# Kernel tuning notes

Hardware: AMD Instinct MI355X
Metric: run time of the kernel (lower is better)

Reference implementation:

```python
import jax, jax.numpy as jnp
import numpy as np
from jax.scipy.linalg import solve_triangular

EPS = 2e-05  # module eps (only used on Cholesky failure in torch; cov is PD here since M >> N)


def setup_inputs() -> dict:
    key = jax.random.key(0)
    k1, k2, k3 = jax.random.split(key, 3)
    B, N, H, W = 8, 512, 64, 64
    return {
        "cont_feat": jax.random.normal(k1, (B, N, H, W), dtype=jnp.float32),
        "styl_feat": jax.random.normal(k2, (B, N, H, W), dtype=jnp.float32),
        "x_real": jax.random.normal(k3, (B, N, H, W), dtype=jnp.float32),
    }


def reference(cont_feat, styl_feat, x_real):
    B, N, cH, cW = cont_feat.shape
    xc = cont_feat.reshape(B, N, -1)   # [B, N, Mc]
    xs = styl_feat.reshape(B, N, -1)   # [B, N, Ms]
    # x_real is reshaped in the original but never used by whitening()

    # whitening: center, covariance, Cholesky, inv(L) @ x (as triangular solve)
    xc_c = xc - jnp.mean(xc, axis=-1, keepdims=True)
    cov_c = jnp.einsum('bnm,bkm->bnk', xc_c, xc_c) / (xc_c.shape[-1] - 1)  # [B,N,N]
    Lc = jnp.linalg.cholesky(cov_c)
    whiten = solve_triangular(Lc, xc_c, lower=True)  # == inv(Lc) @ xc_c

    # coloring: style covariance Cholesky, Ls @ whiten + style mean
    xs_mean = jnp.mean(xs, axis=-1, keepdims=True)
    xs_c = xs - xs_mean
    cov_s = jnp.einsum('bnm,bkm->bnk', xs_c, xs_c) / (xs_c.shape[-1] - 1)
    Ls = jnp.linalg.cholesky(cov_s)
    out = jnp.einsum('bnk,bkm->bnm', Ls, whiten) + xs_mean
    return out.reshape(B, N, cH, cW)
```

## Files before the change

### kernel.cpp

```cpp
#include <hip/hip_runtime.h>
#include <stdint.h>


using short8   = __attribute__((ext_vector_type(8))) short;
using short4_t = __attribute__((ext_vector_type(4))) short;
using f32x4    = __attribute__((ext_vector_type(4))) float;

#define DEVI static __device__ __forceinline__

DEVI uint16_t f32_to_bf16(float f) {
  union { float f; uint32_t u; } v{f};
  uint32_t u = v.u;
  return (uint16_t)((u + 0x7fffu + ((u >> 16) & 1u)) >> 16);
}

DEVI f32x4 mfma16(short8 a, short8 b, f32x4 c) {
  return __builtin_amdgcn_mfma_f32_16x16x32_bf16(a, b, c, 0, 0, 0);
}

typedef __attribute__((address_space(3))) uint32_t lds_u32;
typedef __attribute__((address_space(1))) const uint32_t gmem_u32;

DEVI void async_cp16(const uint16_t* g, uint16_t* l) {
  __builtin_amdgcn_global_load_lds((gmem_u32*)g, (lds_u32*)l, 16, 0, 0);
}

DEVI void stage_tile(const uint16_t* __restrict__ src, int stride,
                     uint16_t* lds, int tid) {
  int w64 = (tid >> 6) << 6;
  #pragma unroll
  for (int i = 0; i < 4; ++i) {
    int f = i * 256 + tid;
    int r = f >> 3, s = f & 7;
    int c = s ^ (r & 7);
    async_cp16(src + r * stride + c * 8, lds + (i * 256 + w64) * 8);
  }
}

DEVI short8 frag_ld(const uint16_t* lds, int r, int ch) {
  return *(const short8*)(lds + r * 64 + ((ch ^ (r & 7)) * 8));
}

__global__ __launch_bounds__(256) void k_meanconv(
    const float* __restrict__ cont, const float* __restrict__ styl,
    uint16_t* __restrict__ Yc, uint16_t* __restrict__ Ys, float* __restrict__ mus) {
  int rid = blockIdx.x;
  int row = rid & 4095;
  bool is_s = rid >= 4096;
  const float* src = (is_s ? styl : cont) + (size_t)row * 4096;
  uint16_t* dst = (is_s ? Ys : Yc) + (size_t)row * 4096;
  int tid = threadIdx.x, lane = tid & 63, w = tid >> 6;

  float4 v[4];
  #pragma unroll
  for (int i = 0; i < 4; ++i) v[i] = ((const float4*)src)[i * 256 + tid];
  float s = 0.f;
  #pragma unroll
  for (int i = 0; i < 4; ++i) s += v[i].x + v[i].y + v[i].z + v[i].w;
  #pragma unroll
  for (int off = 32; off > 0; off >>= 1) s += __shfl_down(s, off);
  __shared__ float red[4];
  if (lane == 0) red[w] = s;
  __syncthreads();
  float mean = (red[0] + red[1] + red[2] + red[3]) * (1.0f / 4096.0f);
  if (is_s && tid == 0) mus[row] = mean;

  #pragma unroll
  for (int i = 0; i < 4; ++i) {
    short4_t o;
    o[0] = (short)f32_to_bf16(v[i].x - mean);
    o[1] = (short)f32_to_bf16(v[i].y - mean);
    o[2] = (short)f32_to_bf16(v[i].z - mean);
    o[3] = (short)f32_to_bf16(v[i].w - mean);
    ((short4_t*)dst)[i * 256 + tid] = o;
  }
}

__global__ __launch_bounds__(256) void k_cov(const uint16_t* __restrict__ Y,
                                             float* __restrict__ covA) {
  int bx = blockIdx.x;
  int mat = bx / 10, q = bx % 10;
  int it = (q >= 6) ? 3 : (q >= 3) ? 2 : (q >= 1) ? 1 : 0;
  int jt = q - it * (it + 1) / 2;
  const uint16_t* A = Y + (size_t)mat * 2097152;
  float* C = covA + (size_t)mat * 262144;
  __shared__ uint16_t Al[128 * 64], Bl[128 * 64];
  int tid = threadIdx.x, lane = tid & 63, w = tid >> 6;
  int wr = w >> 1, wc = w & 1, m16 = lane & 15, q4 = lane >> 4;

  f32x4 acc[4][4] = {};
  for (int kb = 0; kb < 64; ++kb) {
    __syncthreads();
    stage_tile(A + it * 128 * 4096 + kb * 64, 4096, Al, tid);
    stage_tile(A + jt * 128 * 4096 + kb * 64, 4096, Bl, tid);
    __syncthreads();
    #pragma unroll
    for (int ks = 0; ks < 2; ++ks) {
      short8 af[4], bg[4];
      #pragma unroll
      for (int t = 0; t < 4; ++t) af[t] = frag_ld(Al, wr * 64 + t * 16 + m16, ks * 4 + q4);
      #pragma unroll
      for (int t = 0; t < 4; ++t) bg[t] = frag_ld(Bl, wc * 64 + t * 16 + m16, ks * 4 + q4);
      #pragma unroll
      for (int i2 = 0; i2 < 4; ++i2)
        #pragma unroll
        for (int j2 = 0; j2 < 4; ++j2)
          acc[i2][j2] = mfma16(af[i2], bg[j2], acc[i2][j2]);
    }
  }
  const float sc = 1.0f / 4095.0f;
  #pragma unroll
  for (int t = 0; t < 4; ++t)
    #pragma unroll
    for (int u = 0; u < 4; ++u)
      #pragma unroll
      for (int g = 0; g < 4; ++g) {
        int row = it * 128 + wr * 64 + t * 16 + q4 * 4 + g;
        int col = jt * 128 + wc * 64 + u * 16 + m16;
        C[row * 512 + col] = acc[t][u][g] * sc;
      }
}

__global__ __launch_bounds__(512) void k_chol(float* __restrict__ covA,
                                              uint16_t* __restrict__ L16) {
  int mat = blockIdx.x;
  float* C = covA + (size_t)mat * 262144;
  uint16_t* L = L16 + (size_t)mat * 262144;
  __shared__ float P[512 * 33];
  __shared__ float invD[32];
  int tid = threadIdx.x, lane = tid & 63, w = tid >> 6;
  int m16 = lane & 15, q4 = lane >> 4;

  for (int j = 0; j < 16; ++j) {
    int c0 = j * 32, n = 512 - c0;
    for (int e = tid; e < n * 32; e += 512) {
      int r = e >> 5, c = e & 31;
      P[r * 33 + c] = C[(c0 + r) * 512 + c0 + c];
    }
    __syncthreads();
    if (j > 0) {
      int ntiles = n >> 4;
      for (int t = w; t < ntiles; t += 8) {
        f32x4 acc0 = {}, acc1 = {};
        for (int kk = 0; kk < c0; kk += 32) {
          short8 a  = *(const short8*)(L + (size_t)(c0 + t * 16 + m16) * 512 + kk + q4 * 8);
          short8 b0 = *(const short8*)(L + (size_t)(c0 + m16) * 512 + kk + q4 * 8);
          short8 b1 = *(const short8*)(L + (size_t)(c0 + 16 + m16) * 512 + kk + q4 * 8);
          acc0 = mfma16(a, b0, acc0);
          acc1 = mfma16(a, b1, acc1);
        }
        #pragma unroll
        for (int g = 0; g < 4; ++g) {
          int r = t * 16 + q4 * 4 + g;
          P[r * 33 + m16]      -= acc0[g];
          P[r * 33 + 16 + m16] -= acc1[g];
        }
      }
    }
    __syncthreads();
    if (w == 0 && lane < 32) {
      int r = lane;
      float a[32];
      #pragma unroll
      for (int c = 0; c < 32; ++c) a[c] = P[r * 33 + c];
      #pragma unroll
      for (int t = 0; t < 32; ++t) {
        float pv  = __shfl(a[t], t);
        float inv = __builtin_amdgcn_rsqf(pv);
        a[t] *= inv;
        if (r == 0) invD[t] = inv;
        float scv = a[t];
        #pragma unroll
        for (int c = t + 1; c < 32; ++c)
          a[c] -= scv * __shfl(scv, c);
      }
      #pragma unroll
      for (int c = 0; c < 32; ++c) P[r * 33 + c] = a[c];
    }
    __syncthreads();
    if (n > 32) {
      int r = 32 + tid;
      if (r < n) {
        float x[32];
        #pragma unroll
        for (int c = 0; c < 32; ++c) x[c] = P[r * 33 + c];
        #pragma unroll
        for (int c = 0; c < 32; ++c) {
          float s = x[c];
          #pragma unroll
          for (int m = 0; m < c; ++m) s -= x[m] * P[c * 33 + m];
          x[c] = s * invD[c];
        }
        #pragma unroll
        for (int c = 0; c < 32; ++c) P[r * 33 + c] = x[c];
      }
      __syncthreads();
    }
    for (int e = tid; e < n * 32; e += 512) {
      int r = e >> 5, c = e & 31;
      float v2 = P[r * 33 + c];
      if (r < 32 && c > r) v2 = 0.0f;
      C[(c0 + r) * 512 + c0 + c] = v2;
      L[(c0 + r) * 512 + c0 + c] = f32_to_bf16(v2);
    }
    __syncthreads();
  }
}

__global__ __launch_bounds__(256) void k_trinv(const float* __restrict__ covA,
                                               uint16_t* __restrict__ Ut) {
  int bx = blockIdx.x;
  int matb = bx >> 5;
  int sub = bx & 31;
  int cb = sub >> 2, colgrp = sub & 3;
  const float* Lm = covA + (size_t)matb * 262144;
  uint16_t* U = Ut + (size_t)matb * 262144;
  int tid = threadIdx.x, lane = tid & 63, w = tid >> 6;
  int j = cb * 64 + colgrp * 16 + w * 4;

  __shared__ float Bl[64 * 66];
  __shared__ float Xl[4][4][512];

  for (int rb = cb; rb < 8; ++rb) {
    float acc[4];
    #pragma unroll
    for (int c = 0; c < 4; ++c) acc[c] = ((rb * 64 + lane) == (j + c)) ? 1.0f : 0.0f;
    for (int pb = cb; pb < rb; ++pb) {
      __syncthreads();
      for (int e = tid; e < 4096; e += 256)
        Bl[(e >> 6) * 66 + (e & 63)] = Lm[(rb * 64 + (e >> 6)) * 512 + pb * 64 + (e & 63)];
      __syncthreads();
      #pragma unroll 4
      for (int m = 0; m < 64; m += 2) {
        float2 b2 = *(const float2*)&Bl[lane * 66 + m];
        #pragma unroll
        for (int c = 0; c < 4; ++c)
          acc[c] -= b2.x * Xl[w][c][pb * 64 + m] + b2.y * Xl[w][c][pb * 64 + m + 1];
      }
    }
    __syncthreads();
    for (int e = tid; e < 4096; e += 256)
      Bl[(e >> 6) * 66 + (e & 63)] = Lm[(rb * 64 + (e >> 6)) * 512 + rb * 64 + (e & 63)];
    __syncthreads();
    float invd = __builtin_amdgcn_rcpf(Bl[lane * 66 + lane]);
    #pragma unroll 1
    for (int i = 0; i < 64; ++i) {
      float bcol = Bl[lane * 66 + i];
      if (lane == i) {
        #pragma unroll
        for (int c = 0; c < 4; ++c) acc[c] *= invd;
      }
      float xi[4];
      #pragma unroll
      for (int c = 0; c < 4; ++c) xi[c] = __shfl(acc[c], i);
      if (lane > i) {
        #pragma unroll
        for (int c = 0; c < 4; ++c) acc[c] -= bcol * xi[c];
      }
    }
    #pragma unroll
    for (int c = 0; c < 4; ++c) {
      Xl[w][c][rb * 64 + lane] = acc[c];
      U[(j + c) * 512 + rb * 64 + lane] = f32_to_bf16(acc[c]);
    }
  }
}

__global__ __launch_bounds__(256) void k_tprod(const uint16_t* __restrict__ Ls16,
                                               const uint16_t* __restrict__ Ut16,
                                               uint16_t* __restrict__ T16) {
  int bx = blockIdx.x;
  int b = bx / 10, q = bx % 10;
  int it = (q >= 6) ? 3 : (q >= 3) ? 2 : (q >= 1) ? 1 : 0;
  int jt = q - it * (it + 1) / 2;
  const uint16_t* A = Ls16 + (size_t)b * 262144;
  const uint16_t* B = Ut16 + (size_t)b * 262144;
  uint16_t* C = T16 + (size_t)b * 262144;
  __shared__ uint16_t Al[128 * 64], Bl[128 * 64];
  int tid = threadIdx.x, lane = tid & 63, w = tid >> 6;
  int wr = w >> 1, wc = w & 1, m16 = lane & 15, q4 = lane >> 4;

  f32x4 acc[4][4] = {};
  for (int kb = jt * 2; kb < (it + 1) * 2; ++kb) {
    __syncthreads();
    stage_tile(A + it * 128 * 512 + kb * 64, 512, Al, tid);
    stage_tile(B + jt * 128 * 512 + kb * 64, 512, Bl, tid);
    __syncthreads();
    #pragma unroll
    for (int ks = 0; ks < 2; ++ks) {
      short8 af[4], bg[4];
      #pragma unroll
      for (int t = 0; t < 4; ++t) af[t] = frag_ld(Al, wr * 64 + t * 16 + m16, ks * 4 + q4);
      #pragma unroll
      for (int t = 0; t < 4; ++t) bg[t] = frag_ld(Bl, wc * 64 + t * 16 + m16, ks * 4 + q4);
      #pragma unroll
      for (int i2 = 0; i2 < 4; ++i2)
        #pragma unroll
        for (int j2 = 0; j2 < 4; ++j2)
          acc[i2][j2] = mfma16(af[i2], bg[j2], acc[i2][j2]);
    }
  }
  #pragma unroll
  for (int t = 0; t < 4; ++t)
    #pragma unroll
    for (int u = 0; u < 4; ++u)
      #pragma unroll
      for (int g = 0; g < 4; ++g) {
        int row = it * 128 + wr * 64 + t * 16 + q4 * 4 + g;
        int col = jt * 128 + wc * 64 + u * 16 + m16;
        C[row * 512 + col] = f32_to_bf16(acc[t][u][g]);
      }
}

__global__ __launch_bounds__(256) void k_out(const uint16_t* __restrict__ T16,
                                             const uint16_t* __restrict__ Ycb,
                                             const float* __restrict__ mus,
                                             float* __restrict__ out) {
  int bx = blockIdx.x;
  int b = bx >> 7, q = bx & 127;
  int it = q >> 5, mt = q & 31;
  int m0 = mt * 128;
  const uint16_t* Tm = T16 + (size_t)b * 262144;
  const uint16_t* Y = Ycb + (size_t)b * 2097152;
  __shared__ uint16_t Al[128 * 64];
  __shared__ uint16_t Bt[128 * 68];
  int tid = threadIdx.x, lane = tid & 63, w = tid >> 6;
  int wr = w >> 1, wc = w & 1, m16 = lane & 15, q4 = lane >> 4;

  f32x4 acc[4][4] = {};
  int kbmax = (it + 1) * 2;
  for (int kb = 0; kb < kbmax; ++kb) {
    __syncthreads();
    stage_tile(Tm + it * 128 * 512 + kb * 64, 512, Al, tid);
    #pragma unroll
    for (int rep = 0; rep < 2; ++rep) {
      int task = rep * 256 + tid;
      int n8 = task & 15, kp = task >> 4;
      const uint16_t* p = Y + (size_t)(kb * 64 + 2 * kp) * 4096 + m0 + n8 * 8;
      short8 a0 = *(const short8*)p;
      short8 a1 = *(const short8*)(p + 4096);
      #pragma unroll
      for (int u = 0; u < 8; ++u) {
        int n = n8 * 8 + u;
        uint32_t pk = (uint32_t)(uint16_t)a0[u] | ((uint32_t)(uint16_t)a1[u] << 16);
        *(uint32_t*)(Bt + n * 68 + 2 * kp) = pk;
      }
    }
    __syncthreads();
    #pragma unroll
    for (int ks = 0; ks < 2; ++ks) {
      short8 af[4], bg[4];
      #pragma unroll
      for (int t = 0; t < 4; ++t) af[t] = frag_ld(Al, wr * 64 + t * 16 + m16, ks * 4 + q4);
      #pragma unroll
      for (int t = 0; t < 4; ++t) {
        int n = wc * 64 + t * 16 + m16;
        int ko = ks * 4 + q4;
        short8 bb;
        ((short4_t*)&bb)[0] = *(const short4_t*)(Bt + n * 68 + ko * 8);
        ((short4_t*)&bb)[1] = *(const short4_t*)(Bt + n * 68 + ko * 8 + 4);
        bg[t] = bb;
      }
      #pragma unroll
      for (int i2 = 0; i2 < 4; ++i2)
        #pragma unroll
        for (int j2 = 0; j2 < 4; ++j2)
          acc[i2][j2] = mfma16(af[i2], bg[j2], acc[i2][j2]);
    }
  }
  #pragma unroll
  for (int t = 0; t < 4; ++t)
    #pragma unroll
    for (int g = 0; g < 4; ++g) {
      int row = it * 128 + wr * 64 + t * 16 + q4 * 4 + g;
      float mu = mus[b * 512 + row];
      #pragma unroll
      for (int u = 0; u < 4; ++u) {
        int col = m0 + wc * 64 + u * 16 + m16;
        out[(size_t)(b * 512 + row) * 4096 + col] = acc[t][u][g] + mu;
      }
    }
}

extern "C" void kernel_launch(void* const* d_in, const int* in_sizes, int n_in,
                              void* d_out, int out_size, void* d_ws, size_t ws_size,
                              hipStream_t stream) {
  const float* cont = (const float*)d_in[0];
  const float* styl = (const float*)d_in[1];
  float* out = (float*)d_out;
  char* ws = (char*)d_ws;

  uint16_t* Ycb  = (uint16_t*)(ws);
  float*    covA = (float*)(ws + 67108864);
  uint16_t* L16  = (uint16_t*)(ws + 83886080);
  uint16_t* Ut16 = (uint16_t*)(ws + 92274688);
  uint16_t* T16  = (uint16_t*)(ws + 96468992);
  float*    mus  = (float*)(ws + 100663296);

  uint16_t* Ysb  = Ycb + 16777216;
  uint16_t* Ls16 = L16 + 8 * 262144;

  hipMemsetAsync((void*)L16, 0, 16777216, stream);

  k_meanconv<<<dim3(8192), dim3(256), 0, stream>>>(cont, styl, Ycb, Ysb, mus);
  k_cov     <<<dim3(160),  dim3(256), 0, stream>>>(Ycb, covA);
  k_chol    <<<dim3(16),   dim3(512), 0, stream>>>(covA, L16);
  k_trinv   <<<dim3(256),  dim3(256), 0, stream>>>(covA, Ut16);
  k_tprod   <<<dim3(80),   dim3(256), 0, stream>>>(Ls16, Ut16, T16);
  k_out     <<<dim3(1024), dim3(256), 0, stream>>>(T16, Ycb, mus, out);
}
```

Measured before the change: 849.4 us.

## Restructure blocked Cholesky into right-looking rank-32 updates overlapped with diagonal factorization

The Cholesky kernel moves from a left-looking scheme, which recomputed the full trailing GEMM from global bf16 L each panel, to a right-looking scheme. After each panel, the trailing matrix gets a rank-32 update using a bf16 copy of the panel kept in LDS. The next panel's columns are precomputed into shared memory, so wave 0 can factor the diagonal block while the other waves apply the trailing update, with the block size doubled to 1024 threads. The triangular panel solve uses vectorized LDS reads and two rows per thread. This removes the redundant O(n^2·k) reloads of L per panel, but adds read-modify-write traffic on the fp32 trailing matrix in global memory and accumulates bf16 rounding across updates.

```diff
diff --git a/kernel.cpp b/kernel.cpp
--- a/kernel.cpp
+++ b/kernel.cpp
@@ -121,87 +121,190 @@
       }
 }
 
-__global__ __launch_bounds__(512) void k_chol(float* __restrict__ covA,
-                                              uint16_t* __restrict__ L16) {
+__global__ __launch_bounds__(1024) void k_chol(float* __restrict__ covA,
+                                               uint16_t* __restrict__ L16) {
   int mat = blockIdx.x;
   float* C = covA + (size_t)mat * 262144;
   uint16_t* L = L16 + (size_t)mat * 262144;
-  __shared__ float P[512 * 33];
+  __shared__ float P[512 * 36];
+  __shared__ uint16_t Pb[512 * 40];
   __shared__ float invD[32];
   int tid = threadIdx.x, lane = tid & 63, w = tid >> 6;
   int m16 = lane & 15, q4 = lane >> 4;
 
+  for (int e = tid; e < 4096; e += 1024) {
+    int r = e >> 3, c4 = e & 7;
+    *(float4*)&P[r * 36 + c4 * 4] = *(const float4*)(C + r * 512 + c4 * 4);
+  }
+  __syncthreads();
+
   for (int j = 0; j < 16; ++j) {
     int c0 = j * 32, n = 512 - c0;
-    for (int e = tid; e < n * 32; e += 512) {
-      int r = e >> 5, c = e & 31;
-      P[r * 33 + c] = C[(c0 + r) * 512 + c0 + c];
-    }
-    __syncthreads();
-    if (j > 0) {
-      int ntiles = n >> 4;
-      for (int t = w; t < ntiles; t += 8) {
-        f32x4 acc0 = {}, acc1 = {};
-        for (int kk = 0; kk < c0; kk += 32) {
-          short8 a  = *(const short8*)(L + (size_t)(c0 + t * 16 + m16) * 512 + kk + q4 * 8);
-          short8 b0 = *(const short8*)(L + (size_t)(c0 + m16) * 512 + kk + q4 * 8);
-          short8 b1 = *(const short8*)(L + (size_t)(c0 + 16 + m16) * 512 + kk + q4 * 8);
-          acc0 = mfma16(a, b0, acc0);
-          acc1 = mfma16(a, b1, acc1);
-        }
-        #pragma unroll
-        for (int g = 0; g < 4; ++g) {
-          int r = t * 16 + q4 * 4 + g;
-          P[r * 33 + m16]      -= acc0[g];
-          P[r * 33 + 16 + m16] -= acc1[g];
-        }
-      }
-    }
-    __syncthreads();
-    if (w == 0 && lane < 32) {
+
+    if (w == 0) {
+      if (lane < 32) {
+        int r = lane;
+        float a[32];
+        #pragma unroll
+        for (int c4 = 0; c4 < 8; ++c4) {
+          float4 v = *(const float4*)&P[r * 36 + c4 * 4];
+          a[c4 * 4 + 0] = v.x; a[c4 * 4 + 1] = v.y;
+          a[c4 * 4 + 2] = v.z; a[c4 * 4 + 3] = v.w;
+        }
+        #pragma unroll
+        for (int t = 0; t < 32; ++t) {
+          float pv  = __shfl(a[t], t);
+          float inv = __builtin_amdgcn_rsqf(pv);
+          a[t] *= inv;
+          if (r == 0) invD[t] = inv;
+          float scv = a[t];
+          #pragma unroll
+          for (int c = t + 1; c < 32; ++c)
+            a[c] -= scv * __shfl(scv, c);
+        }
+        #pragma unroll
+        for (int c = 0; c < 32; ++c) P[r * 36 + c] = a[c];
+      }
+    } else if (j > 0) {
+      int m = n - 32;
+      if (m > 0) {
+        int nt = m >> 4;
+        int Ttot = (nt * (nt + 1)) >> 1;
+        int base = c0 + 32;
+        #pragma unroll 2
+        for (int l = w - 1; l < Ttot; l += 15) {
+          int ti = (int)((sqrtf(8.f * (float)l + 1.f) - 1.f) * 0.5f);
+          while (((ti + 1) * (ti + 2)) >> 1 <= l) ++ti;
+          while ((ti * (ti + 1)) >> 1 > l) --ti;
+          int tj = l - ((ti * (ti + 1)) >> 1);
+          short8 afr = *(const short8*)(Pb + (64 + ti * 16 + m16) * 40 + q4 * 8);
+          short8 bfr = *(const short8*)(Pb + (64 + tj * 16 + m16) * 40 + q4 * 8);
+          f32x4 acc = {};
+          acc = mfma16(afr, bfr, acc);
+          float* Cp = C + (size_t)(base + ti * 16 + q4 * 4) * 512 + base + tj * 16 + m16;
+          float v0 = Cp[0], v1 = Cp[512], v2 = Cp[1024], v3 = Cp[1536];
+          Cp[0]    = v0 - acc[0];
+          Cp[512]  = v1 - acc[1];
+          Cp[1024] = v2 - acc[2];
+          Cp[1536] = v3 - acc[3];
+        }
+      }
+    }
+    __syncthreads();
+
+    if (w >= 1 && w <= 4) {
+      int idx = (w - 1) * 64 + lane;
+      int cnt = n - 32;
+      bool h1 = idx < cnt;
+      int r2i = idx + 256;
+      bool h2 = r2i < cnt;
+      if (h1) {
+        int r1 = 32 + idx;
+        int r2 = 32 + (h2 ? r2i : idx);
+        float x1[32], x2[32];
+        #pragma unroll
+        for (int c4 = 0; c4 < 8; ++c4) {
+          float4 va = *(const float4*)&P[r1 * 36 + c4 * 4];
+          float4 vb = *(const float4*)&P[r2 * 36 + c4 * 4];
+          x1[c4 * 4 + 0] = va.x; x1[c4 * 4 + 1] = va.y;
+          x1[c4 * 4 + 2] = va.z; x1[c4 * 4 + 3] = va.w;
+          x2[c4 * 4 + 0] = vb.x; x2[c4 * 4 + 1] = vb.y;
+          x2[c4 * 4 + 2] = vb.z; x2[c4 * 4 + 3] = vb.w;
+        }
+        #pragma unroll
+        for (int c = 0; c < 32; ++c) {
+          float s1 = x1[c], s2 = x2[c];
+          #pragma unroll
+          for (int mq = 0; mq < 32; mq += 4) {
+            if (mq < c) {
+              float4 lc = *(const float4*)&P[c * 36 + mq];
+              if (mq + 0 < c) { s1 -= x1[mq + 0] * lc.x; s2 -= x2[mq + 0] * lc.x; }
+              if (mq + 1 < c) { s1 -= x1[mq + 1] * lc.y; s2 -= x2[mq + 1] * lc.y; }
+              if (mq + 2 < c) { s1 -= x1[mq + 2] * lc.z; s2 -= x2[mq + 2] * lc.z; }
+              if (mq + 3 < c) { s1 -= x1[mq + 3] * lc.w; s2 -= x2[mq + 3] * lc.w; }
+            }
+          }
+          float iv = invD[c];
+          x1[c] = s1 * iv;
+          x2[c] = s2 * iv;
+        }
+        {
+          float* Cw = C + (size_t)(c0 + r1) * 512 + c0;
+          uint16_t* Lw = L + (size_t)(c0 + r1) * 512 + c0;
+          uint16_t* Pw = Pb + r1 * 40;
+          #pragma unroll
+          for (int c4 = 0; c4 < 8; ++c4)
+            *(float4*)(Cw + c4 * 4) = make_float4(x1[c4 * 4], x1[c4 * 4 + 1],
+                                                  x1[c4 * 4 + 2], x1[c4 * 4 + 3]);
+          #pragma unroll
+          for (int c8 = 0; c8 < 4; ++c8) {
+            short8 o;
+            #pragma unroll
+            for (int u = 0; u < 8; ++u) o[u] = (short)f32_to_bf16(x1[c8 * 8 + u]);
+            *(short8*)(Lw + c8 * 8) = o;
+            *(short8*)(Pw + c8 * 8) = o;
+          }
+        }
+        if (h2) {
+          int r2g = 32 + r2i;
+          float* Cw = C + (size_t)(c0 + r2g) * 512 + c0;
+          uint16_t* Lw = L + (size_t)(c0 + r2g) * 512 + c0;
+          uint16_t* Pw = Pb + r2g * 40;
+          #pragma unroll
+          for (int c4 = 0; c4 < 8; ++c4)
+            *(float4*)(Cw + c4 * 4) = make_float4(x2[c4 * 4], x2[c4 * 4 + 1],
+                                                  x2[c4 * 4 + 2], x2[c4 * 4 + 3]);
+          #pragma unroll
+          for (int c8 = 0; c8 < 4; ++c8) {
+            short8 o;
+            #pragma unroll
+            for (int u = 0; u < 8; ++u) o[u] = (short)f32_to_bf16(x2[c8 * 8 + u]);
+            *(short8*)(Lw + c8 * 8) = o;
+            *(short8*)(Pw + c8 * 8) = o;
+          }
+        }
+      }
+    } else if (w == 0 && lane < 32) {
       int r = lane;
-      float a[32];
-      #pragma unroll
-      for (int c = 0; c < 32; ++c) a[c] = P[r * 33 + c];
-      #pragma unroll
-      for (int t = 0; t < 32; ++t) {
-        float pv  = __shfl(a[t], t);
-        float inv = __builtin_amdgcn_rsqf(pv);
-        a[t] *= inv;
-        if (r == 0) invD[t] = inv;
-        float scv = a[t];
-        #pragma unroll
-        for (int c = t + 1; c < 32; ++c)
-          a[c] -= scv * __shfl(scv, c);
-      }
-      #pragma unroll
-      for (int c = 0; c < 32; ++c) P[r * 33 + c] = a[c];
-    }
-    __syncthreads();
-    if (n > 32) {
-      int r = 32 + tid;
-      if (r < n) {
-        float x[32];
-        #pragma unroll
-        for (int c = 0; c < 32; ++c) x[c] = P[r * 33 + c];
-        #pragma unroll
-        for (int c = 0; c < 32; ++c) {
-          float s = x[c];
-          #pragma unroll
-          for (int m = 0; m < c; ++m) s -= x[m] * P[c * 33 + m];
-          x[c] = s * invD[c];
-        }
-        #pragma unroll
-        for (int c = 0; c < 32; ++c) P[r * 33 + c] = x[c];
-      }
-      __syncthreads();
-    }
-    for (int e = tid; e < n * 32; e += 512) {
-      int r = e >> 5, c = e & 31;
-      float v2 = P[r * 33 + c];
-      if (r < 32 && c > r) v2 = 0.0f;
-      C[(c0 + r) * 512 + c0 + c] = v2;
-      L[(c0 + r) * 512 + c0 + c] = f32_to_bf16(v2);
+      float xv[32];
+      #pragma unroll
+      for (int c = 0; c < 32; ++c) xv[c] = (c <= r) ? P[r * 36 + c] : 0.0f;
+      float* Cw = C + (size_t)(c0 + r) * 512 + c0;
+      uint16_t* Lw = L + (size_t)(c0 + r) * 512 + c0;
+      uint16_t* Pw = Pb + r * 40;
+      #pragma unroll
+      for (int c4 = 0; c4 < 8; ++c4)
+        *(float4*)(Cw + c4 * 4) = make_float4(xv[c4 * 4], xv[c4 * 4 + 1],
+                                              xv[c4 * 4 + 2], xv[c4 * 4 + 3]);
+      #pragma unroll
+      for (int c8 = 0; c8 < 4; ++c8) {
+        short8 o;
+        #pragma unroll
+        for (int u = 0; u < 8; ++u) o[u] = (short)f32_to_bf16(xv[c8 * 8 + u]);
+        *(short8*)(Lw + c8 * 8) = o;
+        *(short8*)(Pw + c8 * 8) = o;
+      }
+    }
+    __syncthreads();
+
+    if (j < 15) {
+      int rows2 = (n - 32) >> 4;
+      int T4 = rows2 * 2;
+      #pragma unroll 2
+      for (int t = w; t < T4; t += 16) {
+        int ti = t >> 1, tjc = t & 1;
+        short8 afr = *(const short8*)(Pb + (32 + ti * 16 + m16) * 40 + q4 * 8);
+        short8 bfr = *(const short8*)(Pb + (32 + tjc * 16 + m16) * 40 + q4 * 8);
+        f32x4 acc = {};
+        acc = mfma16(afr, bfr, acc);
+        const float* Cr = C + (size_t)(c0 + 32 + ti * 16 + q4 * 4) * 512
+                            + (c0 + 32 + tjc * 16 + m16);
+        float* Pn = &P[(ti * 16 + q4 * 4) * 36 + tjc * 16 + m16];
+        Pn[0]       = Cr[0]    - acc[0];
+        Pn[36]      = Cr[512]  - acc[1];
+        Pn[72]      = Cr[1024] - acc[2];
+        Pn[108]     = Cr[1536] - acc[3];
+      }
     }
     __syncthreads();
   }
@@ -404,7 +507,7 @@
 
   k_meanconv<<<dim3(8192), dim3(256), 0, stream>>>(cont, styl, Ycb, Ysb, mus);
   k_cov     <<<dim3(160),  dim3(256), 0, stream>>>(Ycb, covA);
-  k_chol    <<<dim3(16),   dim3(512), 0, stream>>>(covA, L16);
+  k_chol    <<<dim3(16),   dim3(1024), 0, stream>>>(covA, L16);
   k_trinv   <<<dim3(256),  dim3(256), 0, stream>>>(covA, Ut16);
   k_tprod   <<<dim3(80),   dim3(256), 0, stream>>>(Ls16, Ut16, T16);
   k_out     <<<dim3(1024), dim3(256), 0, stream>>>(T16, Ycb, mus, out);
```

Measured after the change: 1.200 ms. +41.3%, slower.

## Restructure blocked Cholesky: overlap diagonal factor with panel update, MFMA-based panel solve

Applied to the files above, without the earlier changes.

Wave 0 updates and factors the 32x32 diagonal block and forms its explicit inverse, while the other seven waves compute the trailing panel update concurrently. The per-row scalar triangular solve of the panel is replaced by one bf16 MFMA multiply with the inverted diagonal block. Row-blocked vector loads and stores replace the element-wise copies, and one barrier is removed per step. This cuts serialized scalar work and barriers in a single-block-per-matrix kernel, but the panel is now rounded to bf16 before the solve, which lowers the precision of the L factor.

```diff
diff --git a/kernel.cpp b/kernel.cpp
--- a/kernel.cpp
+++ b/kernel.cpp
@@ -126,84 +126,148 @@
   int mat = blockIdx.x;
   float* C = covA + (size_t)mat * 262144;
   uint16_t* L = L16 + (size_t)mat * 262144;
-  __shared__ float P[512 * 33];
-  __shared__ float invD[32];
+  __shared__ float P[512 * 36];
+  __shared__ uint16_t Pb[512 * 40];
+  __shared__ uint16_t Mb[32 * 40];
   int tid = threadIdx.x, lane = tid & 63, w = tid >> 6;
   int m16 = lane & 15, q4 = lane >> 4;
 
   for (int j = 0; j < 16; ++j) {
     int c0 = j * 32, n = 512 - c0;
-    for (int e = tid; e < n * 32; e += 512) {
-      int r = e >> 5, c = e & 31;
-      P[r * 33 + c] = C[(c0 + r) * 512 + c0 + c];
-    }
-    __syncthreads();
-    if (j > 0) {
-      int ntiles = n >> 4;
+
+    for (int e = tid; e < n * 8; e += 512) {
+      int r = e >> 3, c4 = e & 7;
+      *(float4*)&P[r * 36 + c4 * 4] =
+          *(const float4*)(C + (size_t)(c0 + r) * 512 + c0 + c4 * 4);
+    }
+    __syncthreads();
+
+    if (w == 0) {
+      if (c0 > 0) {
+        f32x4 t00 = {}, t10 = {}, t11 = {};
+        const uint16_t* L0 = L + (size_t)(c0 + m16) * 512;
+        const uint16_t* L1r = L + (size_t)(c0 + 16 + m16) * 512;
+        for (int kk = 0; kk < c0; kk += 32) {
+          short8 f0 = *(const short8*)(L0 + kk + q4 * 8);
+          short8 f1 = *(const short8*)(L1r + kk + q4 * 8);
+          t00 = mfma16(f0, f0, t00);
+          t10 = mfma16(f1, f0, t10);
+          t11 = mfma16(f1, f1, t11);
+        }
+        #pragma unroll
+        for (int g = 0; g < 4; ++g) {
+          int r0 = q4 * 4 + g;
+          P[r0 * 36 + m16]              -= t00[g];
+          P[(16 + r0) * 36 + m16]       -= t10[g];
+          P[(16 + r0) * 36 + 16 + m16]  -= t11[g];
+        }
+      }
+      if (lane < 32) {
+        int r = lane;
+        float a[32];
+        #pragma unroll
+        for (int c4 = 0; c4 < 8; ++c4) {
+          float4 v = *(const float4*)&P[r * 36 + c4 * 4];
+          a[c4 * 4 + 0] = v.x; a[c4 * 4 + 1] = v.y;
+          a[c4 * 4 + 2] = v.z; a[c4 * 4 + 3] = v.w;
+        }
+        float myinv = 0.f;
+        #pragma unroll
+        for (int t = 0; t < 32; ++t) {
+          float pv  = __shfl(a[t], t);
+          float inv = __builtin_amdgcn_rsqf(pv);
+          a[t] *= inv;
+          if (r == t) myinv = inv;
+          float scv = a[t];
+          #pragma unroll
+          for (int c = t + 1; c < 32; ++c)
+            a[c] -= scv * __shfl(scv, c);
+        }
+        float xv[32];
+        #pragma unroll
+        for (int c = 0; c < 32; ++c) xv[c] = (c <= r) ? a[c] : 0.0f;
+        float* Cw = C + (size_t)(c0 + r) * 512 + c0;
+        uint16_t* Lw = L + (size_t)(c0 + r) * 512 + c0;
+        #pragma unroll
+        for (int c4 = 0; c4 < 8; ++c4)
+          *(float4*)(Cw + c4 * 4) = make_float4(xv[c4 * 4], xv[c4 * 4 + 1],
+                                                xv[c4 * 4 + 2], xv[c4 * 4 + 3]);
+        #pragma unroll
+        for (int c8 = 0; c8 < 4; ++c8) {
+          short8 o;
+          #pragma unroll
+          for (int u = 0; u < 8; ++u) o[u] = (short)f32_to_bf16(xv[c8 * 8 + u]);
+          *(short8*)(Lw + c8 * 8) = o;
+        }
+        if (n > 32) {
+          float b[32];
+          #pragma unroll
+          for (int c = 0; c < 32; ++c) b[c] = (c == r) ? myinv : 0.0f;
+          #pragma unroll
+          for (int m = 0; m < 31; ++m) {
+            float coef = a[m] * myinv;
+            #pragma unroll
+            for (int c = 0; c <= m; ++c) {
+              float v = __shfl(b[c], m);
+              if (r > m) b[c] -= coef * v;
+            }
+          }
+          uint16_t* Mw = Mb + r * 40;
+          #pragma unroll
+          for (int c8 = 0; c8 < 4; ++c8) {
+            short8 o;
+            #pragma unroll
+            for (int u = 0; u < 8; ++u) o[u] = (short)f32_to_bf16(b[c8 * 8 + u]);
+            *(short8*)(Mw + c8 * 8) = o;
+          }
+        }
+      }
+    } else {
+      int ntiles = (n - 32) >> 4;
+      const uint16_t* B0 = L + (size_t)(c0 + m16) * 512;
+      const uint16_t* B1 = L + (size_t)(c0 + 16 + m16) * 512;
+      for (int t = w - 1; t < ntiles; t += 7) {
+        f32x4 acc0 = {}, acc1 = {};
+        const uint16_t* Ar = L + (size_t)(c0 + 32 + t * 16 + m16) * 512;
+        for (int kk = 0; kk < c0; kk += 32) {
+          short8 af = *(const short8*)(Ar + kk + q4 * 8);
+          short8 b0 = *(const short8*)(B0 + kk + q4 * 8);
+          short8 b1 = *(const short8*)(B1 + kk + q4 * 8);
+          acc0 = mfma16(af, b0, acc0);
+          acc1 = mfma16(af, b1, acc1);
+        }
+        #pragma unroll
+        for (int g = 0; g < 4; ++g) {
+          int pr = 32 + t * 16 + q4 * 4 + g;
+          float v0 = P[pr * 36 + m16]      - acc0[g];
+          float v1 = P[pr * 36 + 16 + m16] - acc1[g];
+          Pb[pr * 40 + m16]      = f32_to_bf16(v0);
+          Pb[pr * 40 + 16 + m16] = f32_to_bf16(v1);
+        }
+      }
+    }
+    __syncthreads();
+
+    if (n > 32) {
+      int ntiles = (n - 32) >> 4;
+      short8 bm0 = *(const short8*)(Mb + m16 * 40 + q4 * 8);
+      short8 bm1 = *(const short8*)(Mb + (16 + m16) * 40 + q4 * 8);
       for (int t = w; t < ntiles; t += 8) {
-        f32x4 acc0 = {}, acc1 = {};
-        for (int kk = 0; kk < c0; kk += 32) {
-          short8 a  = *(const short8*)(L + (size_t)(c0 + t * 16 + m16) * 512 + kk + q4 * 8);
-          short8 b0 = *(const short8*)(L + (size_t)(c0 + m16) * 512 + kk + q4 * 8);
-          short8 b1 = *(const short8*)(L + (size_t)(c0 + 16 + m16) * 512 + kk + q4 * 8);
-          acc0 = mfma16(a, b0, acc0);
-          acc1 = mfma16(a, b1, acc1);
-        }
+        short8 af = *(const short8*)(Pb + (size_t)(32 + t * 16 + m16) * 40 + q4 * 8);
+        f32x4 x0 = {}, x1 = {};
+        x0 = mfma16(af, bm0, x0);
+        x1 = mfma16(af, bm1, x1);
         #pragma unroll
         for (int g = 0; g < 4; ++g) {
-          int r = t * 16 + q4 * 4 + g;
-          P[r * 33 + m16]      -= acc0[g];
-          P[r * 33 + 16 + m16] -= acc1[g];
-        }
-      }
-    }
-    __syncthreads();
-    if (w == 0 && lane < 32) {
-      int r = lane;
-      float a[32];
-      #pragma unroll
-      for (int c = 0; c < 32; ++c) a[c] = P[r * 33 + c];
-      #pragma unroll
-      for (int t = 0; t < 32; ++t) {
-        float pv  = __shfl(a[t], t);
-        float inv = __builtin_amdgcn_rsqf(pv);
-        a[t] *= inv;
-        if (r == 0) invD[t] = inv;
-        float scv = a[t];
-        #pragma unroll
-        for (int c = t + 1; c < 32; ++c)
-          a[c] -= scv * __shfl(scv, c);
-      }
-      #pragma unroll
-      for (int c = 0; c < 32; ++c) P[r * 33 + c] = a[c];
-    }
-    __syncthreads();
-    if (n > 32) {
-      int r = 32 + tid;
-      if (r < n) {
-        float x[32];
-        #pragma unroll
-        for (int c = 0; c < 32; ++c) x[c] = P[r * 33 + c];
-        #pragma unroll
-        for (int c = 0; c < 32; ++c) {
-          float s = x[c];
-          #pragma unroll
-          for (int m = 0; m < c; ++m) s -= x[m] * P[c * 33 + m];
-          x[c] = s * invD[c];
-        }
-        #pragma unroll
-        for (int c = 0; c < 32; ++c) P[r * 33 + c] = x[c];
-      }
-      __syncthreads();
-    }
-    for (int e = tid; e < n * 32; e += 512) {
-      int r = e >> 5, c = e & 31;
-      float v2 = P[r * 33 + c];
-      if (r < 32 && c > r) v2 = 0.0f;
-      C[(c0 + r) * 512 + c0 + c] = v2;
-      L[(c0 + r) * 512 + c0 + c] = f32_to_bf16(v2);
-    }
-    __syncthreads();
+          int gr = c0 + 32 + t * 16 + q4 * 4 + g;
+          float v0 = x0[g], v1 = x1[g];
+          C[(size_t)gr * 512 + c0 + m16]      = v0;
+          C[(size_t)gr * 512 + c0 + 16 + m16] = v1;
+          L[(size_t)gr * 512 + c0 + m16]      = f32_to_bf16(v0);
+          L[(size_t)gr * 512 + c0 + 16 + m16] = f32_to_bf16(v1);
+        }
+      }
+    }
   }
 }
 
```

After: 726.8 us. -14.4%, faster.
